# Optimization experiments

Measured on AMD Instinct MI355X. Metric: run time of the kernel, lower is better.

Reference implementation:

```python
import jax, jax.numpy as jnp
import numpy as np
import math

FACTOR = 1

def setup_inputs() -> dict:
    key = jax.random.key(0)
    k1, k2, k3 = jax.random.split(key, 3)
    B, L, V, H, E = 4, 96, 207, 8, 64
    return {
        "queries": jax.random.normal(k1, (B, L, V, H, E), dtype=jnp.float32),
        "keys": jax.random.normal(k2, (B, L, V, H, E), dtype=jnp.float32),
        "values": jax.random.normal(k3, (B, L, V, H, E), dtype=jnp.float32),
    }

def reference(queries, keys, values):
    B, L, V, H, E = queries.shape
    # L == S here; torch code truncates keys/values to length L
    keys = keys[:, :L]
    values = values[:, :L]
    # [B,L,V,H,E] -> [B,H,E,V,L]
    q = jnp.transpose(queries, (0, 3, 4, 2, 1))
    k = jnp.transpose(keys, (0, 3, 4, 2, 1))
    v = jnp.transpose(values, (0, 3, 4, 2, 1))
    # period-based dependency discovery via FFT cross-correlation
    q_fft = jnp.fft.rfft(q, axis=-1)
    k_fft = jnp.fft.rfft(k, axis=-1)
    corr = jnp.fft.irfft(q_fft * jnp.conj(k_fft), n=L, axis=-1)  # [B,H,E,V,L]

    top_k = int(FACTOR * math.log(L))  # static: L is a trace-time constant
    mean_value = corr.mean(axis=1).mean(axis=1)  # [B,V,L]
    # training branch: indices from batch-mean correlation
    global_mean = mean_value.mean(axis=0)  # [V,L]
    _, index = jax.lax.top_k(global_mean, top_k)  # [V,K]
    weights = jnp.take_along_axis(
        mean_value, jnp.broadcast_to(index[None], (B, V, top_k)), axis=-1
    )  # [B,V,K]
    tmp_corr = jax.nn.softmax(weights, axis=-1)  # [B,V,K]

    # time-delay aggregation: weighted sum of per-vertex rolled values.
    # Loop over small fixed top_k (=4) to avoid the [B,H,E,V,L,K] blowup.
    l_idx = jnp.arange(L)
    agg = jnp.zeros_like(v)
    for kk in range(top_k):
        idxmat = (l_idx[None, :] + index[:, kk:kk + 1]) % L  # [V,L]
        rolled = jnp.take_along_axis(v, idxmat[None, None, None], axis=-1)  # [B,H,E,V,L]
        agg = agg + rolled * tmp_corr[:, None, None, :, kk:kk + 1]
    # [B,H,E,V,L] -> [B,L,V,E,H] (matches torch permute(0,4,3,2,1))
    return jnp.transpose(agg, (0, 4, 3, 2, 1))
```

## Files before the change

### kernel.cpp

```cpp
#include <hip/hip_runtime.h>

#define B 4
#define L 96
#define V 207
#define H 8
#define E 64
#define C 512
#define LS (V*C)
#define TOPK 4
#define QPAD 68
#define TPAD 128

#define MV_OFF 0
#define IDX_OFF (B*V*L*4)
#define TC_OFF  (IDX_OFF + V*TOPK*4)

typedef float f32x4 __attribute__((ext_vector_type(4)));
typedef _Float16 f16x8 __attribute__((ext_vector_type(8)));

__global__ __launch_bounds__(256) void corr_mean_kernel(
        const float* __restrict__ q, const float* __restrict__ k,
        float* __restrict__ mv) {
    __shared__ __attribute__((aligned(16))) float Qs[L * QPAD];
    __shared__ __attribute__((aligned(16))) float Ks[L * QPAD];
    __shared__ float corr[L];

    const int bid = blockIdx.x;
    const int b = bid / V;
    const int v = bid % V;
    const int tid = threadIdx.x;
    const int lane = tid & 63;
    const int wave = tid >> 6;
    const int lrow = lane & 15;
    const int lq = lane >> 4;
    const int rbase = (wave >> 1) * 48;
    const int cbase = (wave & 1) * 48;

    const size_t base = ((size_t)b * L * V + v) * (size_t)C;

    f32x4 acc[3][3];
#pragma unroll
    for (int i = 0; i < 3; i++)
#pragma unroll
        for (int j = 0; j < 3; j++) acc[i][j] = (f32x4){0.f, 0.f, 0.f, 0.f};

    for (int c0 = 0; c0 < C; c0 += 64) {
#pragma unroll
        for (int it = 0; it < 6; it++) {
            const int id = tid + it * 256;
            const int t = id >> 4;
            const int s = id & 15;
            const size_t g = base + (size_t)t * LS + c0 + s * 4;
            const float4 qv = *(const float4*)(q + g);
            const float4 kv = *(const float4*)(k + g);
            *(float4*)(Qs + t * QPAD + s * 4) = qv;
            *(float4*)(Ks + t * QPAD + s * 4) = kv;
        }
        __syncthreads();

#pragma unroll
        for (int kk = 0; kk < 2; kk++) {
            const int soff = kk * 32 + lq * 8;
            f16x8 qh[3], ql[3], kh[3], kl[3];
#pragma unroll
            for (int ti = 0; ti < 3; ti++) {
                const int t = rbase + ti * 16 + lrow;
                const float* p = Qs + t * QPAD + soff;
                const float4 a0 = *(const float4*)(p);
                const float4 a1 = *(const float4*)(p + 4);
                const float xs[8] = {a0.x, a0.y, a0.z, a0.w,
                                     a1.x, a1.y, a1.z, a1.w};
#pragma unroll
                for (int j = 0; j < 8; j++) {
                    const _Float16 h = (_Float16)xs[j];
                    qh[ti][j] = h;
                    ql[ti][j] = (_Float16)(xs[j] - (float)h);
                }
            }
#pragma unroll
            for (int tj = 0; tj < 3; tj++) {
                const int t = cbase + tj * 16 + lrow;
                const float* p = Ks + t * QPAD + soff;
                const float4 a0 = *(const float4*)(p);
                const float4 a1 = *(const float4*)(p + 4);
                const float xs[8] = {a0.x, a0.y, a0.z, a0.w,
                                     a1.x, a1.y, a1.z, a1.w};
#pragma unroll
                for (int j = 0; j < 8; j++) {
                    const _Float16 h = (_Float16)xs[j];
                    kh[tj][j] = h;
                    kl[tj][j] = (_Float16)(xs[j] - (float)h);
                }
            }
#pragma unroll
            for (int ti = 0; ti < 3; ti++)
#pragma unroll
                for (int tj = 0; tj < 3; tj++) {
                    acc[ti][tj] = __builtin_amdgcn_mfma_f32_16x16x32_f16(
                        qh[ti], kh[tj], acc[ti][tj], 0, 0, 0);
                    acc[ti][tj] = __builtin_amdgcn_mfma_f32_16x16x32_f16(
                        qh[ti], kl[tj], acc[ti][tj], 0, 0, 0);
                    acc[ti][tj] = __builtin_amdgcn_mfma_f32_16x16x32_f16(
                        ql[ti], kh[tj], acc[ti][tj], 0, 0, 0);
                }
        }
        __syncthreads();
    }

    if (tid < L) corr[tid] = 0.f;
    __syncthreads();

#pragma unroll
    for (int d = -2; d <= 2; d++) {
        f32x4 s = (f32x4){0.f, 0.f, 0.f, 0.f};
#pragma unroll
        for (int ti = 0; ti < 3; ti++) {
            const int tj = ti - d;
            if (tj >= 0 && tj < 3) s += acc[ti][tj];
        }
#pragma unroll
        for (int r = 0; r < 4; r++) {
            int tau = rbase - cbase + d * 16 + lq * 4 + r - lrow;
            tau = ((tau % L) + L) % L;
            atomicAdd(&corr[tau], s[r]);
        }
    }
    __syncthreads();

    if (tid < L) mv[((size_t)b * V + v) * L + tid] = corr[tid] * (1.0f / 512.0f);
}

__global__ __launch_bounds__(64) void topk_softmax_kernel(
        const float* __restrict__ mv, int* __restrict__ idx,
        float* __restrict__ tc) {
    __shared__ float gm[L];
    __shared__ int sidx[TOPK];
    const int v = blockIdx.x;
    const int tid = threadIdx.x;

    {
        float s0 = 0.f, s1 = 0.f;
#pragma unroll
        for (int b = 0; b < B; b++) {
            s0 += mv[((size_t)b * V + v) * L + tid];
            if (tid < 32) s1 += mv[((size_t)b * V + v) * L + 64 + tid];
        }
        gm[tid] = s0;
        if (tid < 32) gm[64 + tid] = s1;
    }
    __syncthreads();

    for (int kk = 0; kk < TOPK; kk++) {
        float val = gm[tid];
        int id2 = tid;
        if (tid < 32) {
            const float v2 = gm[64 + tid];
            if (v2 > val) { val = v2; id2 = 64 + tid; }
        }
#pragma unroll
        for (int off = 32; off > 0; off >>= 1) {
            const float ov = __shfl_xor(val, off);
            const int oi = __shfl_xor(id2, off);
            if (ov > val || (ov == val && oi < id2)) { val = ov; id2 = oi; }
        }
        if (tid == 0) { sidx[kk] = id2; gm[id2] = -1e30f; }
        __syncthreads();
    }

    if (tid < B) {
        const int b = tid;
        float w[TOPK];
        float m = -1e30f;
#pragma unroll
        for (int kk = 0; kk < TOPK; kk++) {
            w[kk] = mv[((size_t)b * V + v) * L + sidx[kk]];
            m = fmaxf(m, w[kk]);
        }
        float s = 0.f;
#pragma unroll
        for (int kk = 0; kk < TOPK; kk++) { w[kk] = expf(w[kk] - m); s += w[kk]; }
        const float inv = 1.f / s;
#pragma unroll
        for (int kk = 0; kk < TOPK; kk++)
            tc[((size_t)b * V + v) * TOPK + kk] = w[kk] * inv;
    }
    if (tid < TOPK) idx[v * TOPK + tid] = sidx[tid];
}

__global__ __launch_bounds__(256) void agg_kernel(
        const float* __restrict__ val, const float* __restrict__ tc,
        const int* __restrict__ idx, float* __restrict__ out) {
    __shared__ __attribute__((aligned(16))) float T[L * TPAD];
    __shared__ int sidx[TOPK];
    __shared__ float sw[TOPK];

    const int p = blockIdx.x;
    const int bid = (p & 7) * ((B * V * 4) / 8) + (p >> 3);
    const int qtr = bid & 3;
    const int bv = bid >> 2;
    const int b = bv / V;
    const int v = bv % V;
    const int tid = threadIdx.x;
    const int e0 = qtr * 16;

    const size_t base = ((size_t)b * L * V + v) * (size_t)C;

    if (tid < TOPK) {
        sidx[tid] = idx[v * TOPK + tid];
        sw[tid] = tc[((size_t)b * V + v) * TOPK + tid];
    }

#pragma unroll
    for (int it = 0; it < 12; it++) {
        const int id = tid + it * 256;
        const int l = id >> 5;
        const int h = (id & 31) >> 2;
        const int f4 = id & 3;
        const float4 r = *(const float4*)(val + base + (size_t)l * LS + h * 64 + e0 + f4 * 4);
        float* dst = T + l * TPAD + f4 * 32 + h;
        dst[(0 ^ f4) * 8] = r.x;
        dst[(1 ^ f4) * 8] = r.y;
        dst[(2 ^ f4) * 8] = r.z;
        dst[(3 ^ f4) * 8] = r.w;
    }
    __syncthreads();

    const float w0 = sw[0], w1 = sw[1], w2 = sw[2], w3 = sw[3];
    const int i0 = sidx[0], i1 = sidx[1], i2 = sidx[2], i3 = sidx[3];

#pragma unroll
    for (int it = 0; it < 12; it++) {
        const int id = tid + it * 256;
        const int l = id >> 5;
        const int m = id & 31;
        const int f4 = m >> 3;
        const int w = m & 7;
        const int off = f4 * 32 + (((((w >> 1) ^ f4) << 1) | (w & 1)) << 2);
        int l0 = l + i0; if (l0 >= L) l0 -= L;
        int l1 = l + i1; if (l1 >= L) l1 -= L;
        int l2 = l + i2; if (l2 >= L) l2 -= L;
        int l3 = l + i3; if (l3 >= L) l3 -= L;
        const float4 r0 = *(const float4*)(T + l0 * TPAD + off);
        const float4 r1 = *(const float4*)(T + l1 * TPAD + off);
        const float4 r2 = *(const float4*)(T + l2 * TPAD + off);
        const float4 r3 = *(const float4*)(T + l3 * TPAD + off);
        float4 o;
        o.x = w0 * r0.x + w1 * r1.x + w2 * r2.x + w3 * r3.x;
        o.y = w0 * r0.y + w1 * r1.y + w2 * r2.y + w3 * r3.y;
        o.z = w0 * r0.z + w1 * r1.z + w2 * r2.z + w3 * r3.z;
        o.w = w0 * r0.w + w1 * r1.w + w2 * r2.w + w3 * r3.w;
        *(float4*)(out + base + (size_t)l * LS + qtr * 128 + m * 4) = o;
    }
}

extern "C" void kernel_launch(void* const* d_in, const int* in_sizes, int n_in,
                              void* d_out, int out_size, void* d_ws, size_t ws_size,
                              hipStream_t stream) {
    const float* q = (const float*)d_in[0];
    const float* k = (const float*)d_in[1];
    const float* val = (const float*)d_in[2];
    float* out = (float*)d_out;
    char* ws = (char*)d_ws;
    float* mv = (float*)(ws + MV_OFF);
    int* idx = (int*)(ws + IDX_OFF);
    float* tc = (float*)(ws + TC_OFF);

    corr_mean_kernel<<<B * V, 256, 0, stream>>>(q, k, mv);
    topk_softmax_kernel<<<V, 64, 0, stream>>>(mv, idx, tc);
    agg_kernel<<<B * V * 4, 256, 0, stream>>>(val, tc, idx, out);
}
```

Measured before the change: 502.1 us.

## Split correlation over channel chunks with atomic reduction, async LDS loads, finer agg blocks

The correlation kernel now splits the 512-channel reduction into 4 chunks across blocks, giving four times as many blocks. Partial means are combined with global atomics into a buffer cleared by a new zero kernel. Q/K tiles are loaded with global_load_lds direct-to-LDS transfers using an XOR swizzle, and fp16 hi/lo splitting uses packed cvt_pkrtz. The aggregation kernel uses 8 E-slices per (b,v), each with a smaller tile and higher occupancy bounds. The cost is an extra launch, atomic contention, and round-toward-zero conversion, which slightly changes the split precision.

After: 536.3 us. +6.8%, slower.

```diff
diff --git a/kernel.cpp b/kernel.cpp
--- a/kernel.cpp
+++ b/kernel.cpp
@@ -8,8 +8,9 @@
 #define C 512
 #define LS (V*C)
 #define TOPK 4
-#define QPAD 68
-#define TPAD 128
+#define CCH 32
+#define NCH 4
+#define TPAD 68
 
 #define MV_OFF 0
 #define IDX_OFF (B*V*L*4)
@@ -17,17 +18,42 @@
 
 typedef float f32x4 __attribute__((ext_vector_type(4)));
 typedef _Float16 f16x8 __attribute__((ext_vector_type(8)));
-
-__global__ __launch_bounds__(256) void corr_mean_kernel(
+typedef __fp16 fp16x2 __attribute__((ext_vector_type(2)));
+
+union F16X8U { f16x8 v; fp16x2 h[4]; };
+
+__device__ __forceinline__ void split_frag(const float4 a, const float4 b,
+                                           f16x8& hi, f16x8& lo) {
+    F16X8U uh, ul;
+    uh.h[0] = __builtin_amdgcn_cvt_pkrtz(a.x, a.y);
+    uh.h[1] = __builtin_amdgcn_cvt_pkrtz(a.z, a.w);
+    uh.h[2] = __builtin_amdgcn_cvt_pkrtz(b.x, b.y);
+    uh.h[3] = __builtin_amdgcn_cvt_pkrtz(b.z, b.w);
+    ul.h[0] = __builtin_amdgcn_cvt_pkrtz(a.x - (float)uh.h[0].x, a.y - (float)uh.h[0].y);
+    ul.h[1] = __builtin_amdgcn_cvt_pkrtz(a.z - (float)uh.h[1].x, a.w - (float)uh.h[1].y);
+    ul.h[2] = __builtin_amdgcn_cvt_pkrtz(b.x - (float)uh.h[2].x, b.y - (float)uh.h[2].y);
+    ul.h[3] = __builtin_amdgcn_cvt_pkrtz(b.z - (float)uh.h[3].x, b.w - (float)uh.h[3].y);
+    hi = uh.v; lo = ul.v;
+}
+
+__global__ __launch_bounds__(256) void zero_mv_kernel(float4* __restrict__ mv4) {
+    const int i = blockIdx.x * 256 + threadIdx.x;
+    if (i < (B * V * L) / 4) mv4[i] = make_float4(0.f, 0.f, 0.f, 0.f);
+}
+
+__global__ __launch_bounds__(256, 4) void corr_mean_kernel(
         const float* __restrict__ q, const float* __restrict__ k,
         float* __restrict__ mv) {
-    __shared__ __attribute__((aligned(16))) float Qs[L * QPAD];
-    __shared__ __attribute__((aligned(16))) float Ks[L * QPAD];
+    __shared__ __attribute__((aligned(16))) float Qs[L * CCH];
+    __shared__ __attribute__((aligned(16))) float Ks[L * CCH];
     __shared__ float corr[L];
 
-    const int bid = blockIdx.x;
-    const int b = bid / V;
-    const int v = bid % V;
+    const int p = blockIdx.x;
+    const int bid = (p & 7) * ((B * V * NCH) / 8) + (p >> 3);
+    const int chunk = bid / (B * V);
+    const int bvi = bid % (B * V);
+    const int b = bvi / V;
+    const int v = bvi % V;
     const int tid = threadIdx.x;
     const int lane = tid & 63;
     const int wave = tid >> 6;
@@ -37,6 +63,13 @@
     const int cbase = (wave & 1) * 48;
 
     const size_t base = ((size_t)b * L * V + v) * (size_t)C;
+    const int cb = chunk * (C / NCH);
+
+    const int trow = lane >> 3;
+    const int srcs = (lane & 7) ^ trow;
+    const int t7 = lrow & 7;
+    const int fo0 = ((2 * lq) ^ t7) << 2;
+    const int fo1 = fo0 ^ 4;
 
     f32x4 acc[3][3];
 #pragma unroll
@@ -44,66 +77,46 @@
 #pragma unroll
         for (int j = 0; j < 3; j++) acc[i][j] = (f32x4){0.f, 0.f, 0.f, 0.f};
 
-    for (int c0 = 0; c0 < C; c0 += 64) {
-#pragma unroll
-        for (int it = 0; it < 6; it++) {
-            const int id = tid + it * 256;
-            const int t = id >> 4;
-            const int s = id & 15;
-            const size_t g = base + (size_t)t * LS + c0 + s * 4;
-            const float4 qv = *(const float4*)(q + g);
-            const float4 kv = *(const float4*)(k + g);
-            *(float4*)(Qs + t * QPAD + s * 4) = qv;
-            *(float4*)(Ks + t * QPAD + s * 4) = kv;
+    for (int jc = 0; jc < (C / NCH) / CCH; jc++) {
+        const int c0 = cb + jc * CCH;
+#pragma unroll
+        for (int i = 0; i < 3; i++) {
+            const int g = wave * 3 + i;
+            const int t = g * 8 + trow;
+            const size_t goff = base + (size_t)t * LS + c0 + srcs * 4;
+            __builtin_amdgcn_global_load_lds(
+                (const __attribute__((address_space(1))) void*)(q + goff),
+                (__attribute__((address_space(3))) void*)(Qs + g * 256), 16, 0, 0);
+            __builtin_amdgcn_global_load_lds(
+                (const __attribute__((address_space(1))) void*)(k + goff),
+                (__attribute__((address_space(3))) void*)(Ks + g * 256), 16, 0, 0);
         }
         __syncthreads();
 
-#pragma unroll
-        for (int kk = 0; kk < 2; kk++) {
-            const int soff = kk * 32 + lq * 8;
-            f16x8 qh[3], ql[3], kh[3], kl[3];
-#pragma unroll
-            for (int ti = 0; ti < 3; ti++) {
-                const int t = rbase + ti * 16 + lrow;
-                const float* p = Qs + t * QPAD + soff;
-                const float4 a0 = *(const float4*)(p);
-                const float4 a1 = *(const float4*)(p + 4);
-                const float xs[8] = {a0.x, a0.y, a0.z, a0.w,
-                                     a1.x, a1.y, a1.z, a1.w};
-#pragma unroll
-                for (int j = 0; j < 8; j++) {
-                    const _Float16 h = (_Float16)xs[j];
-                    qh[ti][j] = h;
-                    ql[ti][j] = (_Float16)(xs[j] - (float)h);
-                }
+        f16x8 qhi[3], qlo[3], khi[3], klo[3];
+#pragma unroll
+        for (int ti = 0; ti < 3; ti++) {
+            const float* pr = Qs + (rbase + ti * 16 + lrow) * CCH;
+            split_frag(*(const float4*)(pr + fo0), *(const float4*)(pr + fo1),
+                       qhi[ti], qlo[ti]);
+        }
+#pragma unroll
+        for (int tj = 0; tj < 3; tj++) {
+            const float* pr = Ks + (cbase + tj * 16 + lrow) * CCH;
+            split_frag(*(const float4*)(pr + fo0), *(const float4*)(pr + fo1),
+                       khi[tj], klo[tj]);
+        }
+#pragma unroll
+        for (int ti = 0; ti < 3; ti++)
+#pragma unroll
+            for (int tj = 0; tj < 3; tj++) {
+                acc[ti][tj] = __builtin_amdgcn_mfma_f32_16x16x32_f16(
+                    qhi[ti], khi[tj], acc[ti][tj], 0, 0, 0);
+                acc[ti][tj] = __builtin_amdgcn_mfma_f32_16x16x32_f16(
+                    qhi[ti], klo[tj], acc[ti][tj], 0, 0, 0);
+                acc[ti][tj] = __builtin_amdgcn_mfma_f32_16x16x32_f16(
+                    qlo[ti], khi[tj], acc[ti][tj], 0, 0, 0);
             }
-#pragma unroll
-            for (int tj = 0; tj < 3; tj++) {
-                const int t = cbase + tj * 16 + lrow;
-                const float* p = Ks + t * QPAD + soff;
-                const float4 a0 = *(const float4*)(p);
-                const float4 a1 = *(const float4*)(p + 4);
-                const float xs[8] = {a0.x, a0.y, a0.z, a0.w,
-                                     a1.x, a1.y, a1.z, a1.w};
-#pragma unroll
-                for (int j = 0; j < 8; j++) {
-                    const _Float16 h = (_Float16)xs[j];
-                    kh[tj][j] = h;
-                    kl[tj][j] = (_Float16)(xs[j] - (float)h);
-                }
-            }
-#pragma unroll
-            for (int ti = 0; ti < 3; ti++)
-#pragma unroll
-                for (int tj = 0; tj < 3; tj++) {
-                    acc[ti][tj] = __builtin_amdgcn_mfma_f32_16x16x32_f16(
-                        qh[ti], kh[tj], acc[ti][tj], 0, 0, 0);
-                    acc[ti][tj] = __builtin_amdgcn_mfma_f32_16x16x32_f16(
-                        qh[ti], kl[tj], acc[ti][tj], 0, 0, 0);
-                    acc[ti][tj] = __builtin_amdgcn_mfma_f32_16x16x32_f16(
-                        ql[ti], kh[tj], acc[ti][tj], 0, 0, 0);
-                }
-        }
         __syncthreads();
     }
 
@@ -127,7 +140,8 @@
     }
     __syncthreads();
 
-    if (tid < L) mv[((size_t)b * V + v) * L + tid] = corr[tid] * (1.0f / 512.0f);
+    if (tid < L)
+        atomicAdd(&mv[((size_t)b * V + v) * L + tid], corr[tid] * (1.0f / 512.0f));
 }
 
 __global__ __launch_bounds__(64) void topk_softmax_kernel(
@@ -187,7 +201,7 @@
     if (tid < TOPK) idx[v * TOPK + tid] = sidx[tid];
 }
 
-__global__ __launch_bounds__(256) void agg_kernel(
+__global__ __launch_bounds__(256, 6) void agg_kernel(
         const float* __restrict__ val, const float* __restrict__ tc,
         const int* __restrict__ idx, float* __restrict__ out) {
     __shared__ __attribute__((aligned(16))) float T[L * TPAD];
@@ -195,13 +209,13 @@
     __shared__ float sw[TOPK];
 
     const int p = blockIdx.x;
-    const int bid = (p & 7) * ((B * V * 4) / 8) + (p >> 3);
-    const int qtr = bid & 3;
-    const int bv = bid >> 2;
+    const int bid = (p & 7) * ((B * V * 8) / 8) + (p >> 3);
+    const int oct = bid & 7;
+    const int bv = bid >> 3;
     const int b = bv / V;
     const int v = bv % V;
     const int tid = threadIdx.x;
-    const int e0 = qtr * 16;
+    const int e0 = oct * 8;
 
     const size_t base = ((size_t)b * L * V + v) * (size_t)C;
 
@@ -211,17 +225,17 @@
     }
 
 #pragma unroll
-    for (int it = 0; it < 12; it++) {
+    for (int it = 0; it < 6; it++) {
         const int id = tid + it * 256;
-        const int l = id >> 5;
-        const int h = (id & 31) >> 2;
-        const int f4 = id & 3;
+        const int l = id >> 4;
+        const int h = (id & 15) >> 1;
+        const int f4 = id & 1;
         const float4 r = *(const float4*)(val + base + (size_t)l * LS + h * 64 + e0 + f4 * 4);
         float* dst = T + l * TPAD + f4 * 32 + h;
-        dst[(0 ^ f4) * 8] = r.x;
-        dst[(1 ^ f4) * 8] = r.y;
-        dst[(2 ^ f4) * 8] = r.z;
-        dst[(3 ^ f4) * 8] = r.w;
+        dst[0]  = r.x;
+        dst[8]  = r.y;
+        dst[16] = r.z;
+        dst[24] = r.w;
     }
     __syncthreads();
 
@@ -229,27 +243,24 @@
     const int i0 = sidx[0], i1 = sidx[1], i2 = sidx[2], i3 = sidx[3];
 
 #pragma unroll
-    for (int it = 0; it < 12; it++) {
+    for (int it = 0; it < 6; it++) {
         const int id = tid + it * 256;
-        const int l = id >> 5;
-        const int m = id & 31;
-        const int f4 = m >> 3;
-        const int w = m & 7;
-        const int off = f4 * 32 + (((((w >> 1) ^ f4) << 1) | (w & 1)) << 2);
+        const int l = id >> 4;
+        const int m = id & 15;
         int l0 = l + i0; if (l0 >= L) l0 -= L;
         int l1 = l + i1; if (l1 >= L) l1 -= L;
         int l2 = l + i2; if (l2 >= L) l2 -= L;
         int l3 = l + i3; if (l3 >= L) l3 -= L;
-        const float4 r0 = *(const float4*)(T + l0 * TPAD + off);
-        const float4 r1 = *(const float4*)(T + l1 * TPAD + off);
-        const float4 r2 = *(const float4*)(T + l2 * TPAD + off);
-        const float4 r3 = *(const float4*)(T + l3 * TPAD + off);
+        const float4 r0 = *(const float4*)(T + l0 * TPAD + m * 4);
+        const float4 r1 = *(const float4*)(T + l1 * TPAD + m * 4);
+        const float4 r2 = *(const float4*)(T + l2 * TPAD + m * 4);
+        const float4 r3 = *(const float4*)(T + l3 * TPAD + m * 4);
         float4 o;
         o.x = w0 * r0.x + w1 * r1.x + w2 * r2.x + w3 * r3.x;
         o.y = w0 * r0.y + w1 * r1.y + w2 * r2.y + w3 * r3.y;
         o.z = w0 * r0.z + w1 * r1.z + w2 * r2.z + w3 * r3.z;
         o.w = w0 * r0.w + w1 * r1.w + w2 * r2.w + w3 * r3.w;
-        *(float4*)(out + base + (size_t)l * LS + qtr * 128 + m * 4) = o;
+        *(float4*)(out + base + (size_t)l * LS + oct * 64 + m * 4) = o;
     }
 }
 
@@ -265,7 +276,8 @@
     int* idx = (int*)(ws + IDX_OFF);
     float* tc = (float*)(ws + TC_OFF);
 
-    corr_mean_kernel<<<B * V, 256, 0, stream>>>(q, k, mv);
+    zero_mv_kernel<<<(B * V * L / 4 + 255) / 256, 256, 0, stream>>>((float4*)mv);
+    corr_mean_kernel<<<B * V * NCH, 256, 0, stream>>>(q, k, mv);
     topk_softmax_kernel<<<V, 64, 0, stream>>>(mv, idx, tc);
-    agg_kernel<<<B * V * 4, 256, 0, stream>>>(val, tc, idx, out);
-}
+    agg_kernel<<<B * V * 8, 256, 0, stream>>>(val, tc, idx, out);
+}
```
